# Optimization experiments

Measured on AMD Instinct MI355X. Metric: run time of the kernel, lower is better.

## Reference

```python
import jax, jax.numpy as jnp
import numpy as np

H = 2  # attention heads (n_heads)


def _time_enc(t, tw, tb):
    # TGN TimeEncode: cos(t * w + b); t [...,] -> [..., T]
    return jnp.cos(t[..., None] * tw + tb)


def _level0(nodes, node_features, memory_tab):
    # memory[src] + node_features[src]
    return memory_tab[nodes] + node_features[nodes]


def _aggregate(l, src_feat, src_te, neigh, ete, efeat, mask,
               Wq, bq, Wk, bk, Wv, bv, Wo, bo, fc1_w, fc1_b, fc2_w, fc2_b):
    # Temporal graph attention (TGN TemporalAttentionLayer) with padding mask.
    N, K, _ = neigh.shape
    Dq = Wq.shape[-1]
    dh = Dq // H
    q_in = jnp.concatenate([src_feat[:, None, :], src_te], axis=-1)   # [N,1,Dq]
    k_in = jnp.concatenate([neigh, ete, efeat], axis=-1)              # [N,K,Dk]
    q = (q_in @ Wq[l] + bq[l]).reshape(N, 1, H, dh)
    k = (k_in @ Wk[l] + bk[l]).reshape(N, K, H, dh)
    v = (k_in @ Wv[l] + bv[l]).reshape(N, K, H, dh)
    scores = jnp.einsum('nqhd,nkhd->nhqk', q, k) / jnp.sqrt(jnp.asarray(dh, q.dtype))
    all_masked = mask.all(axis=-1)                                    # [N]
    # TGN trick: un-mask column 0 for fully-masked rows, zero output later
    eff_mask = mask & ~(all_masked[:, None] & (jnp.arange(K) == 0))
    scores = jnp.where(eff_mask[:, None, None, :], -1e9, scores)
    attn = jax.nn.softmax(scores, axis=-1)
    o = jnp.einsum('nhqk,nkhd->nqhd', attn, v).reshape(N, Dq)
    o = o @ Wo[l] + bo[l]
    o = jnp.where(all_masked[:, None], 0.0, o)
    # MergeLayer: fc2(relu(fc1(cat[attn_out, src_feat])))
    h = jax.nn.relu(jnp.concatenate([o, src_feat], axis=-1) @ fc1_w[l] + fc1_b[l])
    return h @ fc2_w[l] + fc2_b[l]


def setup_inputs() -> dict:
    key = jax.random.key(0)
    ks = jax.random.split(key, 24)
    B, K, Nn, Ne, D, T = 2048, 20, 1_000_000, 1_000_000, 128, 128
    Dq, Dk = D + T, D + T + D
    inp = {}
    inp['node_features'] = jax.random.normal(ks[0], (Nn, D), jnp.float32) * 0.1
    inp['edge_feat_table'] = jax.random.normal(ks[1], (Ne, D), jnp.float32) * 0.1
    inp['memory_tab'] = jax.random.normal(ks[2], (Nn, D), jnp.float32) * 0.1
    inp['timestamps'] = jax.random.uniform(ks[3], (B,), jnp.float32) * 100.0
    inp['etimes_src'] = jax.random.uniform(ks[4], (B, K), jnp.float32) * 100.0
    inp['etimes_nbr'] = jax.random.uniform(ks[5], (B * K, K), jnp.float32) * 100.0
    inp['tw'] = jax.random.normal(ks[6], (T,), jnp.float32)
    inp['tb'] = jax.random.normal(ks[7], (T,), jnp.float32)
    inp['Wq'] = jax.random.normal(ks[8], (2, Dq, Dq), jnp.float32) / np.sqrt(Dq)
    inp['bq'] = jnp.zeros((2, Dq), jnp.float32)
    inp['Wk'] = jax.random.normal(ks[9], (2, Dk, Dq), jnp.float32) / np.sqrt(Dk)
    inp['bk'] = jnp.zeros((2, Dq), jnp.float32)
    inp['Wv'] = jax.random.normal(ks[10], (2, Dk, Dq), jnp.float32) / np.sqrt(Dk)
    inp['bv'] = jnp.zeros((2, Dq), jnp.float32)
    inp['Wo'] = jax.random.normal(ks[11], (2, Dq, Dq), jnp.float32) / np.sqrt(Dq)
    inp['bo'] = jnp.zeros((2, Dq), jnp.float32)
    inp['fc1_w'] = jax.random.normal(ks[12], (2, Dq + D, D), jnp.float32) / np.sqrt(Dq + D)
    inp['fc1_b'] = jnp.zeros((2, D), jnp.float32)
    inp['fc2_w'] = jax.random.normal(ks[13], (2, D, D), jnp.float32) / np.sqrt(D)
    inp['fc2_b'] = jnp.zeros((2, D), jnp.float32)
    inp['source_nodes'] = jax.random.randint(ks[14], (B,), 0, Nn)
    inp['nbrs_src'] = jax.random.randint(ks[15], (B, K), 0, Nn)
    inp['eidx_src'] = jax.random.randint(ks[16], (B, K), 0, Ne)
    inp['nbrs_nbr'] = jax.random.randint(ks[17], (B * K, K), 0, Nn)
    inp['eidx_nbr'] = jax.random.randint(ks[18], (B * K, K), 0, Ne)
    return inp


def reference(node_features, edge_feat_table, memory_tab, timestamps,
              etimes_src, etimes_nbr, tw, tb,
              Wq, bq, Wk, bk, Wv, bv, Wo, bo, fc1_w, fc1_b, fc2_w, fc2_b,
              source_nodes, nbrs_src, eidx_src, nbrs_nbr, eidx_nbr):
    B, K = nbrs_src.shape
    D = node_features.shape[-1]
    params = (Wq, bq, Wk, bk, Wv, bv, Wo, bo, fc1_w, fc1_b, fc2_w, fc2_b)

    def layer1(nodes, ts, nbrs, eidx, etimes):
        # one temporal-attention hop (n_layers == 1 recursion level)
        src = _level0(nodes, node_features, memory_tab)                 # [N,D]
        neigh = _level0(nbrs.reshape(-1), node_features, memory_tab).reshape(*nbrs.shape, D)
        ete = _time_enc(ts[:, None] - etimes, tw, tb)                   # [N,K,T]
        src_te = _time_enc(jnp.zeros((nodes.shape[0], 1), ts.dtype), tw, tb)
        efeat = edge_feat_table[eidx]                                   # [N,K,De]
        mask = nbrs == 0
        return _aggregate(0, src, src_te, neigh, ete, efeat, mask, *params)

    # layer-1 embedding of sources (recursion uses same temporal neighbors)
    src_conv = layer1(source_nodes, timestamps, nbrs_src, eidx_src, etimes_src)  # [B,D]
    # layer-1 embedding of the sources' neighbors
    ts_rep = jnp.repeat(timestamps, K)                                  # [B*K]
    neigh_emb = layer1(nbrs_src.reshape(-1), ts_rep, nbrs_nbr, eidx_nbr, etimes_nbr)
    neigh_emb = neigh_emb.reshape(B, K, D)
    # layer-2 aggregation over the sources' neighbors
    ete = _time_enc(timestamps[:, None] - etimes_src, tw, tb)           # [B,K,T]
    src_te = _time_enc(jnp.zeros((B, 1), timestamps.dtype), tw, tb)
    efeat = edge_feat_table[eidx_src]
    mask = nbrs_src == 0
    return _aggregate(1, src_conv, src_te, neigh_emb, ete, efeat, mask, *params)
```

## Files before the change

kernel.cpp:

```cpp
#include <hip/hip_runtime.h>
#include <hip/hip_bf16.h>

#define NB   2048
#define KN   20
#define DF   128
#define DQ   256
#define DKI  384
#define NR1  43008
#define SCALE 0.08838834764831845f

typedef short s16x8 __attribute__((ext_vector_type(8)));
typedef short s16x4 __attribute__((ext_vector_type(4)));
typedef float f32x4 __attribute__((ext_vector_type(4)));

__device__ __hip_bfloat16 g_S   [(size_t)NR1*256];
__device__ __hip_bfloat16 g_QKH [(size_t)NR1*768];
__device__ __hip_bfloat16 g_CTX [(size_t)NR1*768];
__device__ __hip_bfloat16 g_Ob  [(size_t)NR1*256];
__device__ __hip_bfloat16 g_FC1A[(size_t)NR1*384];
__device__ __hip_bfloat16 g_Hb  [(size_t)NR1*128];
__device__ float          g_out1[(size_t)NR1*DF];
__device__ float          g_Wqk [2*256*768];
__device__ float          g_bqk [2*768];
__device__ unsigned char  g_allm[NR1];
__device__ __hip_bfloat16 g_Bqk[2*196608];
__device__ __hip_bfloat16 g_Bv [4*49152];
__device__ __hip_bfloat16 g_Bo [2*65536];
__device__ __hip_bfloat16 g_B1 [2*49152];
__device__ __hip_bfloat16 g_B2 [2*16384];

__device__ __forceinline__ short f2bf(float v) {
  union { __hip_bfloat16 h; short s; } u; u.h = __float2bfloat16(v); return u.s;
}
__device__ __forceinline__ float2 bfpair(unsigned u) {
  union { unsigned u2; float f; } a, b;
  a.u2 = u << 16;
  b.u2 = u & 0xFFFF0000u;
  float2 r; r.x = a.f; r.y = b.f; return r;
}
__device__ __forceinline__ s16x4 pack4(float x, float y, float z, float w) {
  s16x4 o; o[0]=f2bf(x); o[1]=f2bf(y); o[2]=f2bf(z); o[3]=f2bf(w); return o;
}

__global__ __launch_bounds__(256)
void k_wqk(const float* __restrict__ Wq, const float* __restrict__ Wk,
           const float* __restrict__ bq) {
  int idx = blockIdx.x*256 + threadIdx.x;
  int L = idx / 196608, rem = idx % 196608;
  int n = rem >> 8, co = rem & 255;
  int h = n / 384, i = n - h*384;
  const float* wqp = Wq + (size_t)L*DQ*DQ  + (size_t)co*DQ + h*128;
  const float* wkp = Wk + (size_t)L*DKI*DQ + (size_t)i*DQ  + h*128;
  float acc = 0.f;
  #pragma unroll 4
  for (int c = 0; c < 128; ++c) acc += wqp[c]*wkp[c];
  g_Wqk[(size_t)(L*256 + co)*768 + n] = acc;
  if (co == 0) {
    const float* bqp = bq + L*DQ + h*128;
    float b = 0.f;
    for (int c = 0; c < 128; ++c) b += bqp[c]*wkp[c];
    g_bqk[L*768 + n] = b;
  }
}

__global__ __launch_bounds__(256)
void k_btile(const float* __restrict__ src, int ldsrc, int K, int N,
             __hip_bfloat16* __restrict__ dst) {
  int slot = blockIdx.x*256 + threadIdx.x;
  if (slot >= (K*N)/8) return;
  int cl = slot & 15, t = slot >> 4;
  int kgn = K >> 3;
  int kg = t % kgn, nt = t / kgn;
  int n = nt*16 + cl;
  s16x8 o;
  #pragma unroll
  for (int e = 0; e < 8; ++e) o[e] = f2bf(src[(size_t)(kg*8 + e)*ldsrc + n]);
  *(s16x8*)(dst + (size_t)slot*8) = o;
}

template<int L>
__global__ __launch_bounds__(256)
void k_prep(const float* __restrict__ nf, const float* __restrict__ mem,
            const float* __restrict__ tb,
            const int* __restrict__ srcn, const int* __restrict__ nbs) {
  const int tid = threadIdx.x;
  const int rl = tid >> 5, q = tid & 31, d0 = q*4;
  const int r = blockIdx.x*8 + rl;
  float ax, ay, az, aw;
  if (L == 0) {
    int node = (r < NB) ? srcn[r] : nbs[r - NB];
    float4 x = *(const float4*)(mem + (size_t)node*DF + d0);
    float4 y = *(const float4*)(nf  + (size_t)node*DF + d0);
    ax=x.x+y.x; ay=x.y+y.y; az=x.z+y.z; aw=x.w+y.w;
  } else {
    float4 x = *(const float4*)(g_out1 + (size_t)r*DF + d0);
    ax=x.x; ay=x.y; az=x.z; aw=x.w;
  }
  *(s16x4*)(g_S + (size_t)r*256 + d0) = pack4(ax, ay, az, aw);
  *(s16x4*)(g_S + (size_t)r*256 + 128 + d0) =
      pack4(cosf(tb[d0]), cosf(tb[d0+1]), cosf(tb[d0+2]), cosf(tb[d0+3]));
  *(s16x4*)(g_FC1A + (size_t)r*384 + 256 + d0) = pack4(ax, ay, az, aw);
}

template<int L>
__global__ __launch_bounds__(256, 6)
void k_edge(const float* __restrict__ nf, const float* __restrict__ ef,
            const float* __restrict__ mem, const float* __restrict__ tsv,
            const float* __restrict__ ets, const float* __restrict__ etn,
            const float* __restrict__ tw,  const float* __restrict__ tb,
            const int* __restrict__ nbs, const int* __restrict__ eis,
            const int* __restrict__ nbn, const int* __restrict__ ein,
            const __hip_bfloat16* __restrict__ QKH,
            __hip_bfloat16* __restrict__ CTX)
{
  const int r = blockIdx.x, tid = threadIdx.x;
  const int lane = tid & 63, w = tid >> 6;

  __shared__ int   nd[KN], ei[KN];
  __shared__ float dts[KN];
  __shared__ float s_sh[2][KN];
  __shared__ float aw_sh[2][KN];
  __shared__ float ctxp[4][768];
  __shared__ unsigned mbits_sh;

  int raw_ = 1;
  if (tid < KN) {
    int nd_, ei_; float dt_;
    if (L == 0) {
      if (r < NB) { raw_ = nbs[r*KN+tid]; nd_ = raw_; ei_ = eis[r*KN+tid]; dt_ = tsv[r] - ets[r*KN+tid]; }
      else { int mm = (r-NB)*KN + tid; raw_ = nbn[mm]; nd_ = raw_; ei_ = ein[mm]; dt_ = tsv[(r-NB)/KN] - etn[mm]; }
    } else {
      raw_ = nbs[r*KN+tid]; nd_ = NB + r*KN + tid; ei_ = eis[r*KN+tid]; dt_ = tsv[r] - ets[r*KN+tid];
    }
    nd[tid] = nd_; ei[tid] = ei_; dts[tid] = dt_;
  }
  if (tid < 64) {
    unsigned long long bal = __ballot(tid < KN && raw_ == 0);
    if (tid == 0) {
      unsigned mb = (unsigned)(bal & 0xFFFFFull);
      mbits_sh = mb;
      g_allm[r] = (mb == 0xFFFFFu) ? 1 : 0;
    }
  }

  const __hip_bfloat16* Qr = QKH + (size_t)r*768;
  float2 q0[3], q1[3];
  #pragma unroll
  for (int seg = 0; seg < 3; ++seg) {
    q0[seg] = bfpair(*(const unsigned*)(Qr +       seg*128 + 2*lane));
    q1[seg] = bfpair(*(const unsigned*)(Qr + 384 + seg*128 + 2*lane));
  }
  float2 twr = *(const float2*)(tw + 2*lane);
  float2 tbr = *(const float2*)(tb + 2*lane);
  __syncthreads();

  int   nds[5], eir[5]; float dtr[5];
  #pragma unroll
  for (int e = 0; e < 5; ++e) {
    int m = w*5 + e;
    nds[e] = nd[m]; eir[e] = ei[m]; dtr[e] = dts[m];
  }
  float2 vm[5], vf[5], vef[5];
  #pragma unroll
  for (int e = 0; e < 5; ++e) {
    if (L == 0) {
      vm[e] = *(const float2*)(mem + (size_t)nds[e]*DF + 2*lane);
      vf[e] = *(const float2*)(nf  + (size_t)nds[e]*DF + 2*lane);
    } else {
      vm[e] = *(const float2*)(g_out1 + (size_t)nds[e]*DF + 2*lane);
    }
    vef[e] = *(const float2*)(ef + (size_t)eir[e]*DF + 2*lane);
  }

  float2 vn[5], vt[5];
  #pragma unroll
  for (int e = 0; e < 5; ++e) {
    if (L == 0) { vn[e].x = vm[e].x + vf[e].x; vn[e].y = vm[e].y + vf[e].y; }
    else        vn[e] = vm[e];
    vt[e].x = __cosf(dtr[e]*twr.x + tbr.x);
    vt[e].y = __cosf(dtr[e]*twr.y + tbr.y);
    float p0 = vn[e].x*q0[0].x + vn[e].y*q0[0].y
             + vt[e].x*q0[1].x + vt[e].y*q0[1].y
             + vef[e].x*q0[2].x + vef[e].y*q0[2].y;
    float p1 = vn[e].x*q1[0].x + vn[e].y*q1[0].y
             + vt[e].x*q1[1].x + vt[e].y*q1[1].y
             + vef[e].x*q1[2].x + vef[e].y*q1[2].y;
    #pragma unroll
    for (int off = 1; off < 64; off <<= 1) {
      p0 += __shfl_xor(p0, off);
      p1 += __shfl_xor(p1, off);
    }
    if (lane == 0) { s_sh[0][w*5+e] = p0; s_sh[1][w*5+e] = p1; }
  }
  __syncthreads();

  if (tid < 64) {
    const int h = tid >> 5, mm = tid & 31;
    const unsigned mb = mbits_sh;
    float sc;
    if (mm < KN) sc = ((mb >> mm) & 1u) ? -1e9f : s_sh[h][mm] * SCALE;
    else         sc = -3.0e38f;
    float mx = sc;
    #pragma unroll
    for (int off = 1; off < 32; off <<= 1) mx = fmaxf(mx, __shfl_xor(mx, off));
    float ev = (mm < KN) ? __expf(sc - mx) : 0.f;
    float sum = ev;
    #pragma unroll
    for (int off = 1; off < 32; off <<= 1) sum += __shfl_xor(sum, off);
    if (mm < KN) aw_sh[h][mm] = ev / sum;
  }
  __syncthreads();

  {
    float2 c0n = {0,0}, c0t = {0,0}, c0e = {0,0};
    float2 c1n = {0,0}, c1t = {0,0}, c1e = {0,0};
    #pragma unroll
    for (int e = 0; e < 5; ++e) {
      const int m = w*5 + e;
      const float a0 = aw_sh[0][m], a1 = aw_sh[1][m];
      c0n.x += a0*vn[e].x;  c0n.y += a0*vn[e].y;
      c0t.x += a0*vt[e].x;  c0t.y += a0*vt[e].y;
      c0e.x += a0*vef[e].x; c0e.y += a0*vef[e].y;
      c1n.x += a1*vn[e].x;  c1n.y += a1*vn[e].y;
      c1t.x += a1*vt[e].x;  c1t.y += a1*vt[e].y;
      c1e.x += a1*vef[e].x; c1e.y += a1*vef[e].y;
    }
    *(float2*)&ctxp[w][      2*lane] = c0n;
    *(float2*)&ctxp[w][128 + 2*lane] = c0t;
    *(float2*)&ctxp[w][256 + 2*lane] = c0e;
    *(float2*)&ctxp[w][384 + 2*lane] = c1n;
    *(float2*)&ctxp[w][512 + 2*lane] = c1t;
    *(float2*)&ctxp[w][640 + 2*lane] = c1e;
  }
  __syncthreads();

  #pragma unroll
  for (int it = 0; it < 3; ++it) {
    int o = it*256 + tid;
    float s = ctxp[0][o] + ctxp[1][o] + ctxp[2][o] + ctxp[3][o];
    CTX[(size_t)r*768 + o] = __float2bfloat16(s);
  }
}

template<int KT, bool F32OUT, bool RELU, bool MASK>
__global__ __launch_bounds__(256, 2)
void k_gemm(const __hip_bfloat16* __restrict__ A, int lda,
            const __hip_bfloat16* __restrict__ B, int kgtot, int nblk,
            void* __restrict__ Cout, int ldc,
            const float* __restrict__ bias,
            const unsigned char* __restrict__ mask)
{
  __shared__ __hip_bfloat16 As[2][128*40];
  __shared__ __hip_bfloat16 Bs[2][128*32];
  const int tid  = threadIdx.x;
  const int lane = tid & 63, wid = tid >> 6;
  const int wm = wid >> 1, wn = wid & 1;
  const int rl = lane & 15, kgs = lane >> 4;
  const int bm = blockIdx.x / nblk, bn = blockIdx.x % nblk;

  f32x4 acc[4][4];
  #pragma unroll
  for (int i = 0; i < 4; ++i)
    #pragma unroll
    for (int j = 0; j < 4; ++j) acc[i][j] = (f32x4){0.f,0.f,0.f,0.f};

  #define STAGE(T, BUF) {                                                      \
    _Pragma("unroll")                                                          \
    for (int i_ = 0; i_ < 2; ++i_) {                                           \
      int row_ = i_*64 + (tid >> 2), kc_ = (tid & 3)*8;                        \
      s16x8 v_ = *(const s16x8*)(A + (size_t)(bm*128 + row_)*lda + (T)*32 + kc_); \
      *(s16x8*)(&As[BUF][row_*40 + kc_]) = v_;                                 \
    }                                                                          \
    _Pragma("unroll")                                                          \
    for (int i_ = 0; i_ < 2; ++i_) {                                           \
      int slot_ = i_*256 + tid;                                                \
      int nt_ = slot_ >> 6, kg_ = (slot_ >> 4) & 3, cl_ = slot_ & 15;          \
      s16x8 w_ = *(const s16x8*)(B + ((size_t)(bn*8 + nt_)*kgtot + (T)*4 + kg_)*128 + cl_*8); \
      *(s16x8*)(&Bs[BUF][slot_*8]) = w_;                                       \
    } }

  STAGE(0, 0);
  __syncthreads();
  int buf = 0;
  for (int t = 0; t < KT; ++t) {
    if (t < KT-1) STAGE(t+1, buf ^ 1);
    s16x8 af[4], bfm[4];
    #pragma unroll
    for (int mtl = 0; mtl < 4; ++mtl)
      af[mtl] = *(const s16x8*)(&As[buf][(wm*64 + mtl*16 + rl)*40 + kgs*8]);
    #pragma unroll
    for (int ntl = 0; ntl < 4; ++ntl)
      bfm[ntl] = *(const s16x8*)(&Bs[buf][((wn*4 + ntl)*4 + kgs)*128 + rl*8]);
    #pragma unroll
    for (int mtl = 0; mtl < 4; ++mtl)
      #pragma unroll
      for (int ntl = 0; ntl < 4; ++ntl)
        acc[mtl][ntl] = __builtin_amdgcn_mfma_f32_16x16x32_bf16(af[mtl], bfm[ntl], acc[mtl][ntl], 0, 0, 0);
    __syncthreads();
    buf ^= 1;
  }
  #undef STAGE

  #pragma unroll
  for (int mtl = 0; mtl < 4; ++mtl) {
    #pragma unroll
    for (int ntl = 0; ntl < 4; ++ntl) {
      int gcol = bn*128 + wn*64 + ntl*16 + rl;
      float bb = bias ? bias[gcol] : 0.f;
      #pragma unroll
      for (int rg = 0; rg < 4; ++rg) {
        int grow = bm*128 + wm*64 + mtl*16 + kgs*4 + rg;
        float v = acc[mtl][ntl][rg] + bb;
        if (RELU) v = fmaxf(v, 0.f);
        if (MASK) { if (mask[grow]) v = 0.f; }
        if (F32OUT) ((float*)Cout)[(size_t)grow*ldc + gcol] = v;
        else ((__hip_bfloat16*)Cout)[(size_t)grow*ldc + gcol] = __float2bfloat16(v);
      }
    }
  }
}

extern "C" void kernel_launch(void* const* d_in, const int* in_sizes, int n_in,
                              void* d_out, int out_size, void* d_ws, size_t ws_size,
                              hipStream_t stream) {
  (void)in_sizes; (void)n_in; (void)out_size; (void)ws_size; (void)d_ws;
  const float* nf   = (const float*)d_in[0];
  const float* ef   = (const float*)d_in[1];
  const float* mem  = (const float*)d_in[2];
  const float* tsv  = (const float*)d_in[3];
  const float* ets  = (const float*)d_in[4];
  const float* etn  = (const float*)d_in[5];
  const float* tw   = (const float*)d_in[6];
  const float* tb   = (const float*)d_in[7];
  const float* Wq   = (const float*)d_in[8];
  const float* bq   = (const float*)d_in[9];
  const float* Wk   = (const float*)d_in[10];
  const float* bv   = (const float*)d_in[13];
  const float* Wv   = (const float*)d_in[12];
  const float* Wo   = (const float*)d_in[14];
  const float* bo   = (const float*)d_in[15];
  const float* f1w  = (const float*)d_in[16];
  const float* f1b  = (const float*)d_in[17];
  const float* f2w  = (const float*)d_in[18];
  const float* f2b  = (const float*)d_in[19];
  const int* srcn   = (const int*)d_in[20];
  const int* nbs    = (const int*)d_in[21];
  const int* eis    = (const int*)d_in[22];
  const int* nbn    = (const int*)d_in[23];
  const int* ein    = (const int*)d_in[24];
  float* out = (float*)d_out;

  __hip_bfloat16 *S, *QKH, *CTX, *Ob, *FC1A, *Hb, *Bqk, *Bv, *Bo, *B1, *B2;
  float *Wqkf, *bqkf, *out1f;
  unsigned char* allm;
  hipGetSymbolAddress((void**)&S,    HIP_SYMBOL(g_S));
  hipGetSymbolAddress((void**)&QKH,  HIP_SYMBOL(g_QKH));
  hipGetSymbolAddress((void**)&CTX,  HIP_SYMBOL(g_CTX));
  hipGetSymbolAddress((void**)&Ob,   HIP_SYMBOL(g_Ob));
  hipGetSymbolAddress((void**)&FC1A, HIP_SYMBOL(g_FC1A));
  hipGetSymbolAddress((void**)&Hb,   HIP_SYMBOL(g_Hb));
  hipGetSymbolAddress((void**)&Bqk,  HIP_SYMBOL(g_Bqk));
  hipGetSymbolAddress((void**)&Bv,   HIP_SYMBOL(g_Bv));
  hipGetSymbolAddress((void**)&Bo,   HIP_SYMBOL(g_Bo));
  hipGetSymbolAddress((void**)&B1,   HIP_SYMBOL(g_B1));
  hipGetSymbolAddress((void**)&B2,   HIP_SYMBOL(g_B2));
  hipGetSymbolAddress((void**)&Wqkf, HIP_SYMBOL(g_Wqk));
  hipGetSymbolAddress((void**)&bqkf, HIP_SYMBOL(g_bqk));
  hipGetSymbolAddress((void**)&out1f,HIP_SYMBOL(g_out1));
  hipGetSymbolAddress((void**)&allm, HIP_SYMBOL(g_allm));

  hipLaunchKernelGGL(k_wqk, dim3(1536), dim3(256), 0, stream, Wq, Wk, bq);
  for (int L = 0; L < 2; ++L) {
    hipLaunchKernelGGL(k_btile, dim3(96), dim3(256), 0, stream, Wqkf + (size_t)L*256*768, 768, 256, 768, Bqk + (size_t)L*196608);
    for (int h = 0; h < 2; ++h)
      hipLaunchKernelGGL(k_btile, dim3(24), dim3(256), 0, stream, Wv + (size_t)L*DKI*DQ + h*128, 256, 384, 128, Bv + (size_t)(L*2+h)*49152);
    hipLaunchKernelGGL(k_btile, dim3(32), dim3(256), 0, stream, Wo + (size_t)L*DQ*DQ,    256, 256, 256, Bo + (size_t)L*65536);
    hipLaunchKernelGGL(k_btile, dim3(24), dim3(256), 0, stream, f1w + (size_t)L*384*128, 128, 384, 128, B1 + (size_t)L*49152);
    hipLaunchKernelGGL(k_btile, dim3(8),  dim3(256), 0, stream, f2w + (size_t)L*128*128, 128, 128, 128, B2 + (size_t)L*16384);
  }

  {
    const int R = NR1, BMg = R/128;
    hipLaunchKernelGGL((k_prep<0>), dim3(R/8), dim3(256), 0, stream, nf, mem, tb, srcn, nbs);
    hipLaunchKernelGGL((k_gemm<8,false,false,false>), dim3(BMg*6), dim3(256), 0, stream,
        S, 256, Bqk, 32, 6, QKH, 768, bqkf, (const unsigned char*)nullptr);
    hipLaunchKernelGGL((k_edge<0>), dim3(R), dim3(256), 0, stream,
        nf, ef, mem, tsv, ets, etn, tw, tb, nbs, eis, nbn, ein, QKH, CTX);
    for (int h = 0; h < 2; ++h)
      hipLaunchKernelGGL((k_gemm<12,false,false,false>), dim3(BMg), dim3(256), 0, stream,
          CTX + h*384, 768, Bv + (size_t)h*49152, 48, 1, Ob + h*128, 256, bv + h*128, (const unsigned char*)nullptr);
    hipLaunchKernelGGL((k_gemm<8,false,false,true>), dim3(BMg*2), dim3(256), 0, stream,
        Ob, 256, Bo, 32, 2, FC1A, 384, bo, allm);
    hipLaunchKernelGGL((k_gemm<12,false,true,false>), dim3(BMg), dim3(256), 0, stream,
        FC1A, 384, B1, 48, 1, Hb, 128, f1b, (const unsigned char*)nullptr);
    hipLaunchKernelGGL((k_gemm<4,true,false,false>), dim3(BMg), dim3(256), 0, stream,
        Hb, 128, B2, 16, 1, out1f, 128, f2b, (const unsigned char*)nullptr);
  }
  {
    const int R = NB, BMg = R/128;
    hipLaunchKernelGGL((k_prep<1>), dim3(R/8), dim3(256), 0, stream, nf, mem, tb, srcn, nbs);
    hipLaunchKernelGGL((k_gemm<8,false,false,false>), dim3(BMg*6), dim3(256), 0, stream,
        S, 256, Bqk + 196608, 32, 6, QKH, 768, bqkf + 768, (const unsigned char*)nullptr);
    hipLaunchKernelGGL((k_edge<1>), dim3(R), dim3(256), 0, stream,
        nf, ef, mem, tsv, ets, etn, tw, tb, nbs, eis, nbn, ein, QKH, CTX);
    for (int h = 0; h < 2; ++h)
      hipLaunchKernelGGL((k_gemm<12,false,false,false>), dim3(BMg), dim3(256), 0, stream,
          CTX + h*384, 768, Bv + (size_t)(2+h)*49152, 48, 1, Ob + h*128, 256, bv + 256 + h*128, (const unsigned char*)nullptr);
    hipLaunchKernelGGL((k_gemm<8,false,false,true>), dim3(BMg*2), dim3(256), 0, stream,
        Ob, 256, Bo + 65536, 32, 2, FC1A, 384, bo + 256, allm);
    hipLaunchKernelGGL((k_gemm<12,false,true,false>), dim3(BMg), dim3(256), 0, stream,
        FC1A, 384, B1 + 49152, 48, 1, Hb, 128, f1b + 128, (const unsigned char*)nullptr);
    hipLaunchKernelGGL((k_gemm<4,true,false,false>), dim3(BMg), dim3(256), 0, stream,
        Hb, 128, B2 + 16384, 16, 1, out, 128, f2b + 128, (const unsigned char*)nullptr);
  }
}
```

Before: 611.2 us.

## Map one wavefront per row in edge attention kernel, removing shared memory and barriers

The edge attention kernel now assigns each 64-lane wavefront a whole row (4 rows per block) instead of spreading one row across four waves. Neighbor metadata moves via lane shuffles, the softmax runs inside the wave, and the context is written straight from registers as packed bf16, so the shared-memory partial sums and the four __syncthreads are gone. The cost is a second gather pass: the neighbor feature rows and the cosine time encodings are reloaded and recomputed for the weighted sum, which adds memory traffic. The launch-bounds occupancy hint also drops from 6 to 4.

```diff
diff --git a/kernel.cpp b/kernel.cpp
--- a/kernel.cpp
+++ b/kernel.cpp
@@ -40,6 +40,9 @@
 }
 __device__ __forceinline__ s16x4 pack4(float x, float y, float z, float w) {
   s16x4 o; o[0]=f2bf(x); o[1]=f2bf(y); o[2]=f2bf(z); o[3]=f2bf(w); return o;
+}
+__device__ __forceinline__ unsigned packbf2(float2 v) {
+  return (unsigned)(unsigned short)f2bf(v.x) | ((unsigned)(unsigned short)f2bf(v.y) << 16);
 }
 
 __global__ __launch_bounds__(256)
@@ -103,7 +106,7 @@
 }
 
 template<int L>
-__global__ __launch_bounds__(256, 6)
+__global__ __launch_bounds__(256, 4)
 void k_edge(const float* __restrict__ nf, const float* __restrict__ ef,
             const float* __restrict__ mem, const float* __restrict__ tsv,
             const float* __restrict__ ets, const float* __restrict__ etn,
@@ -113,35 +116,22 @@
             const __hip_bfloat16* __restrict__ QKH,
             __hip_bfloat16* __restrict__ CTX)
 {
-  const int r = blockIdx.x, tid = threadIdx.x;
+  const int tid = threadIdx.x;
   const int lane = tid & 63, w = tid >> 6;
-
-  __shared__ int   nd[KN], ei[KN];
-  __shared__ float dts[KN];
-  __shared__ float s_sh[2][KN];
-  __shared__ float aw_sh[2][KN];
-  __shared__ float ctxp[4][768];
-  __shared__ unsigned mbits_sh;
-
-  int raw_ = 1;
-  if (tid < KN) {
-    int nd_, ei_; float dt_;
+  const int r = blockIdx.x*4 + w;
+
+  int raw_ = 1, nd_ = 0, ei_ = 0; float dt_ = 0.f;
+  if (lane < KN) {
     if (L == 0) {
-      if (r < NB) { raw_ = nbs[r*KN+tid]; nd_ = raw_; ei_ = eis[r*KN+tid]; dt_ = tsv[r] - ets[r*KN+tid]; }
-      else { int mm = (r-NB)*KN + tid; raw_ = nbn[mm]; nd_ = raw_; ei_ = ein[mm]; dt_ = tsv[(r-NB)/KN] - etn[mm]; }
+      if (r < NB) { raw_ = nbs[r*KN+lane]; nd_ = raw_; ei_ = eis[r*KN+lane]; dt_ = tsv[r] - ets[r*KN+lane]; }
+      else { int mm = (r-NB)*KN + lane; raw_ = nbn[mm]; nd_ = raw_; ei_ = ein[mm]; dt_ = tsv[(r-NB)/KN] - etn[mm]; }
     } else {
-      raw_ = nbs[r*KN+tid]; nd_ = NB + r*KN + tid; ei_ = eis[r*KN+tid]; dt_ = tsv[r] - ets[r*KN+tid];
-    }
-    nd[tid] = nd_; ei[tid] = ei_; dts[tid] = dt_;
-  }
-  if (tid < 64) {
-    unsigned long long bal = __ballot(tid < KN && raw_ == 0);
-    if (tid == 0) {
-      unsigned mb = (unsigned)(bal & 0xFFFFFull);
-      mbits_sh = mb;
-      g_allm[r] = (mb == 0xFFFFFu) ? 1 : 0;
-    }
-  }
+      raw_ = nbs[r*KN+lane]; nd_ = NB + r*KN + lane; ei_ = eis[r*KN+lane]; dt_ = tsv[r] - ets[r*KN+lane];
+    }
+  }
+  unsigned long long bal = __ballot(lane < KN && raw_ == 0);
+  unsigned mb = (unsigned)(bal & 0xFFFFFull);
+  if (lane == 0) g_allm[r] = (mb == 0xFFFFFu) ? 1 : 0;
 
   const __hip_bfloat16* Qr = QKH + (size_t)r*768;
   float2 q0[3], q1[3];
@@ -152,94 +142,115 @@
   }
   float2 twr = *(const float2*)(tw + 2*lane);
   float2 tbr = *(const float2*)(tb + 2*lane);
-  __syncthreads();
-
-  int   nds[5], eir[5]; float dtr[5];
-  #pragma unroll
-  for (int e = 0; e < 5; ++e) {
-    int m = w*5 + e;
-    nds[e] = nd[m]; eir[e] = ei[m]; dtr[e] = dts[m];
-  }
-  float2 vm[5], vf[5], vef[5];
-  #pragma unroll
-  for (int e = 0; e < 5; ++e) {
-    if (L == 0) {
-      vm[e] = *(const float2*)(mem + (size_t)nds[e]*DF + 2*lane);
-      vf[e] = *(const float2*)(nf  + (size_t)nds[e]*DF + 2*lane);
-    } else {
-      vm[e] = *(const float2*)(g_out1 + (size_t)nds[e]*DF + 2*lane);
-    }
-    vef[e] = *(const float2*)(ef + (size_t)eir[e]*DF + 2*lane);
-  }
-
-  float2 vn[5], vt[5];
-  #pragma unroll
-  for (int e = 0; e < 5; ++e) {
-    if (L == 0) { vn[e].x = vm[e].x + vf[e].x; vn[e].y = vm[e].y + vf[e].y; }
-    else        vn[e] = vm[e];
-    vt[e].x = __cosf(dtr[e]*twr.x + tbr.x);
-    vt[e].y = __cosf(dtr[e]*twr.y + tbr.y);
-    float p0 = vn[e].x*q0[0].x + vn[e].y*q0[0].y
-             + vt[e].x*q0[1].x + vt[e].y*q0[1].y
-             + vef[e].x*q0[2].x + vef[e].y*q0[2].y;
-    float p1 = vn[e].x*q1[0].x + vn[e].y*q1[0].y
-             + vt[e].x*q1[1].x + vt[e].y*q1[1].y
-             + vef[e].x*q1[2].x + vef[e].y*q1[2].y;
-    #pragma unroll
-    for (int off = 1; off < 64; off <<= 1) {
-      p0 += __shfl_xor(p0, off);
-      p1 += __shfl_xor(p1, off);
-    }
-    if (lane == 0) { s_sh[0][w*5+e] = p0; s_sh[1][w*5+e] = p1; }
-  }
-  __syncthreads();
-
-  if (tid < 64) {
-    const int h = tid >> 5, mm = tid & 31;
-    const unsigned mb = mbits_sh;
-    float sc;
-    if (mm < KN) sc = ((mb >> mm) & 1u) ? -1e9f : s_sh[h][mm] * SCALE;
-    else         sc = -3.0e38f;
-    float mx = sc;
-    #pragma unroll
-    for (int off = 1; off < 32; off <<= 1) mx = fmaxf(mx, __shfl_xor(mx, off));
-    float ev = (mm < KN) ? __expf(sc - mx) : 0.f;
-    float sum = ev;
-    #pragma unroll
-    for (int off = 1; off < 32; off <<= 1) sum += __shfl_xor(sum, off);
-    if (mm < KN) aw_sh[h][mm] = ev / sum;
-  }
-  __syncthreads();
-
-  {
-    float2 c0n = {0,0}, c0t = {0,0}, c0e = {0,0};
-    float2 c1n = {0,0}, c1t = {0,0}, c1e = {0,0};
-    #pragma unroll
-    for (int e = 0; e < 5; ++e) {
-      const int m = w*5 + e;
-      const float a0 = aw_sh[0][m], a1 = aw_sh[1][m];
-      c0n.x += a0*vn[e].x;  c0n.y += a0*vn[e].y;
-      c0t.x += a0*vt[e].x;  c0t.y += a0*vt[e].y;
-      c0e.x += a0*vef[e].x; c0e.y += a0*vef[e].y;
-      c1n.x += a1*vn[e].x;  c1n.y += a1*vn[e].y;
-      c1t.x += a1*vt[e].x;  c1t.y += a1*vt[e].y;
-      c1e.x += a1*vef[e].x; c1e.y += a1*vef[e].y;
-    }
-    *(float2*)&ctxp[w][      2*lane] = c0n;
-    *(float2*)&ctxp[w][128 + 2*lane] = c0t;
-    *(float2*)&ctxp[w][256 + 2*lane] = c0e;
-    *(float2*)&ctxp[w][384 + 2*lane] = c1n;
-    *(float2*)&ctxp[w][512 + 2*lane] = c1t;
-    *(float2*)&ctxp[w][640 + 2*lane] = c1e;
-  }
-  __syncthreads();
-
-  #pragma unroll
-  for (int it = 0; it < 3; ++it) {
-    int o = it*256 + tid;
-    float s = ctxp[0][o] + ctxp[1][o] + ctxp[2][o] + ctxp[3][o];
-    CTX[(size_t)r*768 + o] = __float2bfloat16(s);
-  }
+
+  float s0r = 0.f, s1r = 0.f;
+  #pragma unroll
+  for (int c0 = 0; c0 < KN; c0 += 5) {
+    int nds[5], eir[5]; float dtr[5];
+    #pragma unroll
+    for (int e = 0; e < 5; ++e) {
+      nds[e] = __shfl(nd_, c0 + e);
+      eir[e] = __shfl(ei_, c0 + e);
+      dtr[e] = __shfl(dt_, c0 + e);
+    }
+    float2 vm[5], vf[5], vef[5];
+    #pragma unroll
+    for (int e = 0; e < 5; ++e) {
+      if (L == 0) {
+        vm[e] = *(const float2*)(mem + (size_t)nds[e]*DF + 2*lane);
+        vf[e] = *(const float2*)(nf  + (size_t)nds[e]*DF + 2*lane);
+      } else {
+        vm[e] = *(const float2*)(g_out1 + (size_t)nds[e]*DF + 2*lane);
+      }
+      vef[e] = *(const float2*)(ef + (size_t)eir[e]*DF + 2*lane);
+    }
+    #pragma unroll
+    for (int e = 0; e < 5; ++e) {
+      float2 vn;
+      if (L == 0) { vn.x = vm[e].x + vf[e].x; vn.y = vm[e].y + vf[e].y; }
+      else        vn = vm[e];
+      float2 vt;
+      vt.x = __cosf(dtr[e]*twr.x + tbr.x);
+      vt.y = __cosf(dtr[e]*twr.y + tbr.y);
+      float p0 = vn.x*q0[0].x + vn.y*q0[0].y + vt.x*q0[1].x + vt.y*q0[1].y
+               + vef[e].x*q0[2].x + vef[e].y*q0[2].y;
+      float p1 = vn.x*q1[0].x + vn.y*q1[0].y + vt.x*q1[1].x + vt.y*q1[1].y
+               + vef[e].x*q1[2].x + vef[e].y*q1[2].y;
+      #pragma unroll
+      for (int off = 1; off < 64; off <<= 1) {
+        p0 += __shfl_xor(p0, off);
+        p1 += __shfl_xor(p1, off);
+      }
+      if (lane == c0 + e) { s0r = p0; s1r = p1; }
+    }
+  }
+
+  float sc0 = (lane < KN) ? (((mb >> lane) & 1u) ? -1e9f : s0r*SCALE) : -3.0e38f;
+  float sc1 = (lane < KN) ? (((mb >> lane) & 1u) ? -1e9f : s1r*SCALE) : -3.0e38f;
+  float mx0 = sc0, mx1 = sc1;
+  #pragma unroll
+  for (int off = 1; off < 64; off <<= 1) {
+    mx0 = fmaxf(mx0, __shfl_xor(mx0, off));
+    mx1 = fmaxf(mx1, __shfl_xor(mx1, off));
+  }
+  float ev0 = (lane < KN) ? __expf(sc0 - mx0) : 0.f;
+  float ev1 = (lane < KN) ? __expf(sc1 - mx1) : 0.f;
+  float su0 = ev0, su1 = ev1;
+  #pragma unroll
+  for (int off = 1; off < 64; off <<= 1) {
+    su0 += __shfl_xor(su0, off);
+    su1 += __shfl_xor(su1, off);
+  }
+  float aw0 = ev0 / su0, aw1 = ev1 / su1;
+
+  float2 c0n = {0,0}, c0t = {0,0}, c0e = {0,0};
+  float2 c1n = {0,0}, c1t = {0,0}, c1e = {0,0};
+  #pragma unroll
+  for (int c0i = 0; c0i < KN; c0i += 5) {
+    int nds[5], eir[5]; float dtr[5], a0[5], a1[5];
+    #pragma unroll
+    for (int e = 0; e < 5; ++e) {
+      nds[e] = __shfl(nd_, c0i + e);
+      eir[e] = __shfl(ei_, c0i + e);
+      dtr[e] = __shfl(dt_, c0i + e);
+      a0[e]  = __shfl(aw0, c0i + e);
+      a1[e]  = __shfl(aw1, c0i + e);
+    }
+    float2 vm[5], vf[5], vef[5];
+    #pragma unroll
+    for (int e = 0; e < 5; ++e) {
+      if (L == 0) {
+        vm[e] = *(const float2*)(mem + (size_t)nds[e]*DF + 2*lane);
+        vf[e] = *(const float2*)(nf  + (size_t)nds[e]*DF + 2*lane);
+      } else {
+        vm[e] = *(const float2*)(g_out1 + (size_t)nds[e]*DF + 2*lane);
+      }
+      vef[e] = *(const float2*)(ef + (size_t)eir[e]*DF + 2*lane);
+    }
+    #pragma unroll
+    for (int e = 0; e < 5; ++e) {
+      float2 vn;
+      if (L == 0) { vn.x = vm[e].x + vf[e].x; vn.y = vm[e].y + vf[e].y; }
+      else        vn = vm[e];
+      float2 vt;
+      vt.x = __cosf(dtr[e]*twr.x + tbr.x);
+      vt.y = __cosf(dtr[e]*twr.y + tbr.y);
+      c0n.x += a0[e]*vn.x;    c0n.y += a0[e]*vn.y;
+      c0t.x += a0[e]*vt.x;    c0t.y += a0[e]*vt.y;
+      c0e.x += a0[e]*vef[e].x; c0e.y += a0[e]*vef[e].y;
+      c1n.x += a1[e]*vn.x;    c1n.y += a1[e]*vn.y;
+      c1t.x += a1[e]*vt.x;    c1t.y += a1[e]*vt.y;
+      c1e.x += a1[e]*vef[e].x; c1e.y += a1[e]*vef[e].y;
+    }
+  }
+
+  unsigned* C32 = (unsigned*)(CTX + (size_t)r*768);
+  C32[0*64 + lane] = packbf2(c0n);
+  C32[1*64 + lane] = packbf2(c0t);
+  C32[2*64 + lane] = packbf2(c0e);
+  C32[3*64 + lane] = packbf2(c1n);
+  C32[4*64 + lane] = packbf2(c1t);
+  C32[5*64 + lane] = packbf2(c1e);
 }
 
 template<int KT, bool F32OUT, bool RELU, bool MASK>
@@ -384,7 +395,7 @@
     hipLaunchKernelGGL((k_prep<0>), dim3(R/8), dim3(256), 0, stream, nf, mem, tb, srcn, nbs);
     hipLaunchKernelGGL((k_gemm<8,false,false,false>), dim3(BMg*6), dim3(256), 0, stream,
         S, 256, Bqk, 32, 6, QKH, 768, bqkf, (const unsigned char*)nullptr);
-    hipLaunchKernelGGL((k_edge<0>), dim3(R), dim3(256), 0, stream,
+    hipLaunchKernelGGL((k_edge<0>), dim3(R/4), dim3(256), 0, stream,
         nf, ef, mem, tsv, ets, etn, tw, tb, nbs, eis, nbn, ein, QKH, CTX);
     for (int h = 0; h < 2; ++h)
       hipLaunchKernelGGL((k_gemm<12,false,false,false>), dim3(BMg), dim3(256), 0, stream,
@@ -401,7 +412,7 @@
     hipLaunchKernelGGL((k_prep<1>), dim3(R/8), dim3(256), 0, stream, nf, mem, tb, srcn, nbs);
     hipLaunchKernelGGL((k_gemm<8,false,false,false>), dim3(BMg*6), dim3(256), 0, stream,
         S, 256, Bqk + 196608, 32, 6, QKH, 768, bqkf + 768, (const unsigned char*)nullptr);
-    hipLaunchKernelGGL((k_edge<1>), dim3(R), dim3(256), 0, stream,
+    hipLaunchKernelGGL((k_edge<1>), dim3(R/4), dim3(256), 0, stream,
         nf, ef, mem, tsv, ets, etn, tw, tb, nbs, eis, nbn, ein, QKH, CTX);
     for (int h = 0; h < 2; ++h)
       hipLaunchKernelGGL((k_gemm<12,false,false,false>), dim3(BMg), dim3(256), 0, stream,
```

Result: slower. 829.9 us (+35.8%).
